# Performance work log

Hardware: AMD Instinct MI355X
Metric: run time of the kernel (lower is better)

## Reference

```python
import jax, jax.numpy as jnp
import numpy as np

SCALE = 0.5
DROP_P = 0.2

def setup_inputs() -> dict:
    key = jax.random.key(0)
    k1, k2 = jax.random.split(key)
    x1 = jax.random.normal(k1, (8, 2048, 128), dtype=jnp.float32)
    x2 = jax.random.normal(k2, (8, 2048, 128), dtype=jnp.float32)
    return {"x1": x1, "x2": x2}

def reference(x1, x2):
    # scores: [B, M, N] = x1 @ x2^T, scaled by 0.5
    scores = jnp.einsum('bmd,bnd->bmn', x1, x2) * SCALE
    probs = jax.nn.softmax(scores, axis=-1)
    # dropout p=0.2 (training mode in the torch source); fixed key for determinism
    keep = jax.random.bernoulli(jax.random.key(42), 1.0 - DROP_P, probs.shape)
    probs = jnp.where(keep, probs / (1.0 - DROP_P), 0.0)
    # out: [B, M, D] = probs @ x2
    return jnp.einsum('bmn,bnd->bmd', probs, x2)
```

## Files before the change

### kernel.cpp

```cpp
#include <hip/hip_runtime.h>
#include <stdint.h>


typedef __bf16 bf16x8 __attribute__((ext_vector_type(8)));
typedef float f32x4 __attribute__((ext_vector_type(4)));

union FragAB {
  bf16x8 v;
  uint32_t u[4];
};

__device__ __forceinline__ uint32_t rotl32(uint32_t x, uint32_t r) {
  return (x << r) | (x >> (32u - r));
}

__device__ __forceinline__ void threefry2x32_k42(uint32_t in0, uint32_t in1,
                                                 uint32_t& o0, uint32_t& o1) {
  const uint32_t ks0 = 0u;
  const uint32_t ks1 = 42u;
  const uint32_t ks2 = 0x1BD11BDAu ^ 0u ^ 42u;
  uint32_t x0 = in0 + ks0;
  uint32_t x1 = in1 + ks1;
#define TFR(r) { x0 += x1; x1 = rotl32(x1, r); x1 ^= x0; }
  TFR(13u) TFR(15u) TFR(26u) TFR(6u)
  x0 += ks1; x1 += ks2 + 1u;
  TFR(17u) TFR(29u) TFR(16u) TFR(24u)
  x0 += ks2; x1 += ks0 + 2u;
  TFR(13u) TFR(15u) TFR(26u) TFR(6u)
  x0 += ks0; x1 += ks1 + 3u;
  TFR(17u) TFR(29u) TFR(16u) TFR(24u)
  x0 += ks1; x1 += ks2 + 4u;
  TFR(13u) TFR(15u) TFR(26u) TFR(6u)
  x0 += ks2; x1 += ks0 + 5u;
#undef TFR
  o0 = x0; o1 = x1;
}

__device__ __forceinline__ uint32_t pack_bf16(float a, float b) {
  __bf16 ba = (__bf16)a;
  __bf16 bb = (__bf16)b;
  uint32_t ua = (uint32_t)__builtin_bit_cast(uint16_t, ba);
  uint32_t ub = (uint32_t)__builtin_bit_cast(uint16_t, bb);
  return ua | (ub << 16);
}

#define KEEP_LT 3435974144u
#define MBIAS 40.0f

__launch_bounds__(256, 4)
__global__ void prep_kernel(const float* __restrict__ x2,
                            uint4* __restrict__ KF,
                            uint4* __restrict__ VF) {
  const int tid = threadIdx.x;
  const int w = tid >> 6;
  const int lane = tid & 63;
  const int l15 = lane & 15;
  const int g = lane >> 4;
  const int T = blockIdx.x;
  const int b = blockIdx.y;
  const float* xb = x2 + (size_t)b * 2048 * 128;

  #pragma unroll
  for (int h = 0; h < 2; ++h) {
    const int n = T * 32 + h * 16 + l15;
    const float* p = xb + (size_t)n * 128 + w * 32 + 8 * g;
    float4 f0 = *(const float4*)(p);
    float4 f1 = *(const float4*)(p + 4);
    uint4 u;
    u.x = pack_bf16(f0.x, f0.y);
    u.y = pack_bf16(f0.z, f0.w);
    u.z = pack_bf16(f1.x, f1.y);
    u.w = pack_bf16(f1.z, f1.w);
    KF[(size_t)((b * 64 + T) * 8 + w * 2 + h) * 64 + lane] = u;
  }

  #pragma unroll
  for (int i = 0; i < 2; ++i) {
    const int dt = w + 4 * i;
    const int d = dt * 16 + l15;
    const float* p = xb + (size_t)(T * 32 + 8 * g) * 128 + d;
    uint4 u;
    u.x = pack_bf16(p[0],   p[128]);
    u.y = pack_bf16(p[256], p[384]);
    u.z = pack_bf16(p[512], p[640]);
    u.w = pack_bf16(p[768], p[896]);
    VF[(size_t)((b * 64 + T) * 8 + dt) * 64 + lane] = u;
  }
}

__launch_bounds__(256, 4)
__global__ void attn2_kernel(const float* __restrict__ x1,
                             const uint4* __restrict__ KF,
                             const uint4* __restrict__ VF,
                             float* __restrict__ out) {
  __shared__ __attribute__((aligned(16))) uint32_t SMEM[8768];

  const int tid = threadIdx.x;
  const int w = __builtin_amdgcn_readfirstlane(tid >> 6);
  const int lane = tid & 63;
  const int l15 = lane & 15;
  const int g = lane >> 4;
  const int id = blockIdx.y * 128 + blockIdx.x;
  const int b = id & 7;
  const int m0 = (id >> 3) * 16;

  uint32_t* PbW = &SMEM[w * 320];

  const float QSCALE = 0.5f * 1.44269504088896340736f;
  FragAB qf[4];
  {
    const float* qp_base = x1 + ((size_t)b * 2048 + m0 + l15) * 128;
    #pragma unroll
    for (int c = 0; c < 4; ++c) {
      const float* qp = qp_base + c * 32 + g * 8;
      float4 f0 = *(const float4*)(qp);
      float4 f1 = *(const float4*)(qp + 4);
      qf[c].u[0] = pack_bf16(f0.x * QSCALE, f0.y * QSCALE);
      qf[c].u[1] = pack_bf16(f0.z * QSCALE, f0.w * QSCALE);
      qf[c].u[2] = pack_bf16(f1.x * QSCALE, f1.y * QSCALE);
      qf[c].u[3] = pack_bf16(f1.z * QSCALE, f1.w * QSCALE);
    }
  }

  f32x4 o[8];
  #pragma unroll
  for (int dt = 0; dt < 8; ++dt) o[dt] = (f32x4){0.f, 0.f, 0.f, 0.f};
  float lsum = 0.f;

  const uint32_t rb = (uint32_t)b * 4194304u +
                      (uint32_t)(m0 + l15) * 2048u + (uint32_t)(w * 512);

  const uint4* kfp = KF + (size_t)((b * 64 + w * 16) * 8) * 64 + lane;
  const uint4* vfp = VF + (size_t)((b * 64 + w * 16) * 8) * 64 + lane;

  uint4 kf[8], vf[8];
  #pragma unroll
  for (int i = 0; i < 8; ++i) kf[i] = kfp[i * 64];

  for (int tile = 0; tile < 16; ++tile) {
    f32x4 sa[2];
    sa[0] = (f32x4){0.f, 0.f, 0.f, 0.f};
    sa[1] = (f32x4){0.f, 0.f, 0.f, 0.f};
    #pragma unroll
    for (int c = 0; c < 4; ++c) {
      FragAB k0, k1;
      k0.u[0] = kf[2 * c].x; k0.u[1] = kf[2 * c].y;
      k0.u[2] = kf[2 * c].z; k0.u[3] = kf[2 * c].w;
      k1.u[0] = kf[2 * c + 1].x; k1.u[1] = kf[2 * c + 1].y;
      k1.u[2] = kf[2 * c + 1].z; k1.u[3] = kf[2 * c + 1].w;
      sa[0] = __builtin_amdgcn_mfma_f32_16x16x32_bf16(k0.v, qf[c].v, sa[0], 0, 0, 0);
      sa[1] = __builtin_amdgcn_mfma_f32_16x16x32_bf16(k1.v, qf[c].v, sa[1], 0, 0, 0);
    }

    #pragma unroll
    for (int i = 0; i < 8; ++i) vf[i] = vfp[i * 64];
    kfp += 512;
    #pragma unroll
    for (int i = 0; i < 8; ++i) kf[i] = kfp[i * 64];

    #pragma unroll
    for (int t = 0; t < 2; ++t) {
      float p0 = __builtin_amdgcn_exp2f(sa[t][0] - MBIAS);
      float p1 = __builtin_amdgcn_exp2f(sa[t][1] - MBIAS);
      float p2 = __builtin_amdgcn_exp2f(sa[t][2] - MBIAS);
      float p3 = __builtin_amdgcn_exp2f(sa[t][3] - MBIAS);
      lsum += (p0 + p1) + (p2 + p3);
      uint32_t ib = rb + (uint32_t)(tile * 32 + t * 16 + 4 * g);
      uint32_t h0, h1, bits;
      threefry2x32_k42(0u, ib + 0u, h0, h1); bits = h0 ^ h1;
      float q0 = (bits < KEEP_LT) ? p0 : 0.0f;
      threefry2x32_k42(0u, ib + 1u, h0, h1); bits = h0 ^ h1;
      float q1 = (bits < KEEP_LT) ? p1 : 0.0f;
      threefry2x32_k42(0u, ib + 2u, h0, h1); bits = h0 ^ h1;
      float q2 = (bits < KEEP_LT) ? p2 : 0.0f;
      threefry2x32_k42(0u, ib + 3u, h0, h1); bits = h0 ^ h1;
      float q3 = (bits < KEEP_LT) ? p3 : 0.0f;
      *(uint2*)&PbW[l15 * 20 + t * 8 + 2 * g] =
          make_uint2(pack_bf16(q0, q1), pack_bf16(q2, q3));
    }
    asm volatile("s_waitcnt lgkmcnt(0)" ::: "memory");
    FragAB pa;
    {
      uint4 pu = *(const uint4*)&PbW[l15 * 20 + 4 * g];
      pa.u[0] = pu.x; pa.u[1] = pu.y; pa.u[2] = pu.z; pa.u[3] = pu.w;
    }

    #pragma unroll
    for (int dt = 0; dt < 8; ++dt) {
      FragAB vb;
      vb.u[0] = vf[dt].x; vb.u[1] = vf[dt].y;
      vb.u[2] = vf[dt].z; vb.u[3] = vf[dt].w;
      o[dt] = __builtin_amdgcn_mfma_f32_16x16x32_bf16(pa.v, vb.v, o[dt], 0, 0, 0);
    }
    vfp += 512;
  }

  __syncthreads();
  float* EP = (float*)&SMEM[0];
  float* EPL = EP + 8192;
  EPL[l15 * 36 + w * 4 + g] = lsum;
  #pragma unroll
  for (int dt = 0; dt < 8; ++dt)
    #pragma unroll
    for (int r = 0; r < 4; ++r)
      EP[((w * 8 + dt) * 4 + r) * 64 + lane] = o[dt][r];
  __syncthreads();
  float scale[4];
  #pragma unroll
  for (int r = 0; r < 4; ++r) {
    const float4* lp = (const float4*)&EPL[(4 * g + r) * 36];
    float4 A = lp[0], B4 = lp[1], C4 = lp[2], D4 = lp[3];
    float L = ((A.x + A.y) + (A.z + A.w)) + ((B4.x + B4.y) + (B4.z + B4.w)) +
              ((C4.x + C4.y) + (C4.z + C4.w)) + ((D4.x + D4.y) + (D4.z + D4.w));
    scale[r] = 1.0f / (L * 0.8f);
  }
  #pragma unroll
  for (int i = 0; i < 2; ++i) {
    const int dt = w * 2 + i;
    #pragma unroll
    for (int r = 0; r < 4; ++r) {
      int base = (dt * 4 + r) * 64 + lane;
      float tot = EP[base] + EP[base + 2048] + EP[base + 4096] + EP[base + 6144];
      out[((size_t)b * 2048 + m0 + 4 * g + r) * 128 + dt * 16 + l15] =
          tot * scale[r];
    }
  }
}

__launch_bounds__(256, 2)
__global__ void attn_kernel(const float* __restrict__ x1,
                            const float* __restrict__ x2,
                            float* __restrict__ out) {
  __shared__ __attribute__((aligned(16))) uint32_t SMEM[4][4800];

  const int tid = threadIdx.x;
  const int wv = __builtin_amdgcn_readfirstlane(tid >> 6);
  const int lane = tid & 63;
  const int l15 = lane & 15;
  const int g = lane >> 4;
  const int b = blockIdx.y;
  const int m0 = blockIdx.x * 32;

  uint32_t* KtW = &SMEM[wv][0];
  uint32_t* VtW = &SMEM[wv][2176];
  uint32_t* PbW = &SMEM[wv][4480];

  const float QSCALE = 0.5f * 1.44269504088896340736f;
  FragAB qf[2][4];
  #pragma unroll
  for (int s = 0; s < 2; ++s) {
    const float* qp_base = x1 + ((size_t)b * 2048 + m0 + s * 16 + l15) * 128;
    #pragma unroll
    for (int c = 0; c < 4; ++c) {
      const float* qp = qp_base + c * 32 + g * 8;
      float4 f0 = *(const float4*)(qp);
      float4 f1 = *(const float4*)(qp + 4);
      qf[s][c].u[0] = pack_bf16(f0.x * QSCALE, f0.y * QSCALE);
      qf[s][c].u[1] = pack_bf16(f0.z * QSCALE, f0.w * QSCALE);
      qf[s][c].u[2] = pack_bf16(f1.x * QSCALE, f1.y * QSCALE);
      qf[s][c].u[3] = pack_bf16(f1.z * QSCALE, f1.w * QSCALE);
    }
  }

  f32x4 o[2][8];
  #pragma unroll
  for (int s = 0; s < 2; ++s)
    #pragma unroll
    for (int dt = 0; dt < 8; ++dt) o[s][dt] = (f32x4){0.f, 0.f, 0.f, 0.f};
  float lsum[2] = {0.f, 0.f};

  uint32_t rb[2];
  #pragma unroll
  for (int s = 0; s < 2; ++s)
    rb[s] = (uint32_t)b * 4194304u +
            (uint32_t)(m0 + s * 16 + l15) * 2048u + (uint32_t)(wv * 512);

  const float4* x2b4 = (const float4*)(x2 + (size_t)b * 2048 * 128);
  const uint32_t permsel = (l15 & 1) ? 0x07060302u : 0x05040100u;

  for (int tile = 0; tile < 16; ++tile) {
    const int n0g = wv * 512 + tile * 32;

    #pragma unroll
    for (int i = 0; i < 16; ++i) {
      int n = 2 * i + (lane >> 5);
      int dq = lane & 31;
      float4 v = x2b4[(size_t)(n0g + n) * 32 + dq];
      uint32_t p0 = pack_bf16(v.x, v.y);
      uint32_t p1 = pack_bf16(v.z, v.w);
      *(uint2*)&KtW[n * 68 + 2 * dq] = make_uint2(p0, p1);
      VtW[dq * 36 + n] = p0;
      VtW[(dq + 32) * 36 + n] = p1;
    }
    asm volatile("s_waitcnt lgkmcnt(0)" ::: "memory");

    f32x4 sa[2][2];
    #pragma unroll
    for (int s = 0; s < 2; ++s)
      #pragma unroll
      for (int t = 0; t < 2; ++t) sa[s][t] = (f32x4){0.f, 0.f, 0.f, 0.f};
    #pragma unroll
    for (int c = 0; c < 4; ++c) {
      FragAB k0, k1;
      uint4 a0 = *(const uint4*)&KtW[l15 * 68 + c * 16 + 4 * g];
      uint4 a1 = *(const uint4*)&KtW[(16 + l15) * 68 + c * 16 + 4 * g];
      k0.u[0] = a0.x; k0.u[1] = a0.y; k0.u[2] = a0.z; k0.u[3] = a0.w;
      k1.u[0] = a1.x; k1.u[1] = a1.y; k1.u[2] = a1.z; k1.u[3] = a1.w;
      sa[0][0] = __builtin_amdgcn_mfma_f32_16x16x32_bf16(k0.v, qf[0][c].v, sa[0][0], 0, 0, 0);
      sa[0][1] = __builtin_amdgcn_mfma_f32_16x16x32_bf16(k1.v, qf[0][c].v, sa[0][1], 0, 0, 0);
      sa[1][0] = __builtin_amdgcn_mfma_f32_16x16x32_bf16(k0.v, qf[1][c].v, sa[1][0], 0, 0, 0);
      sa[1][1] = __builtin_amdgcn_mfma_f32_16x16x32_bf16(k1.v, qf[1][c].v, sa[1][1], 0, 0, 0);
    }

    FragAB pa[2];
    #pragma unroll
    for (int s = 0; s < 2; ++s) {
      #pragma unroll
      for (int t = 0; t < 2; ++t) {
        float p0 = __builtin_amdgcn_exp2f(sa[s][t][0] - MBIAS);
        float p1 = __builtin_amdgcn_exp2f(sa[s][t][1] - MBIAS);
        float p2 = __builtin_amdgcn_exp2f(sa[s][t][2] - MBIAS);
        float p3 = __builtin_amdgcn_exp2f(sa[s][t][3] - MBIAS);
        lsum[s] += (p0 + p1) + (p2 + p3);
        uint32_t ib = rb[s] + (uint32_t)(tile * 32 + t * 16 + 4 * g);
        uint32_t h0, h1, bits;
        threefry2x32_k42(0u, ib + 0u, h0, h1); bits = h0 ^ h1;
        float q0 = (bits < KEEP_LT) ? p0 : 0.0f;
        threefry2x32_k42(0u, ib + 1u, h0, h1); bits = h0 ^ h1;
        float q1 = (bits < KEEP_LT) ? p1 : 0.0f;
        threefry2x32_k42(0u, ib + 2u, h0, h1); bits = h0 ^ h1;
        float q2 = (bits < KEEP_LT) ? p2 : 0.0f;
        threefry2x32_k42(0u, ib + 3u, h0, h1); bits = h0 ^ h1;
        float q3 = (bits < KEEP_LT) ? p3 : 0.0f;
        *(uint2*)&PbW[l15 * 20 + t * 8 + 2 * g] =
            make_uint2(pack_bf16(q0, q1), pack_bf16(q2, q3));
      }
      asm volatile("s_waitcnt lgkmcnt(0)" ::: "memory");
      uint4 pu = *(const uint4*)&PbW[l15 * 20 + 4 * g];
      pa[s].u[0] = pu.x; pa[s].u[1] = pu.y; pa[s].u[2] = pu.z; pa[s].u[3] = pu.w;
    }

    #pragma unroll
    for (int dt = 0; dt < 8; ++dt) {
      int rowp = ((l15 >> 1) & 1) * 32 + 4 * dt + (l15 >> 2);
      const uint32_t* vr = &VtW[rowp * 36 + 8 * g];
      uint4 U0 = *(const uint4*)vr;
      uint4 U1 = *(const uint4*)(vr + 4);
      FragAB vb;
      vb.u[0] = __builtin_amdgcn_perm(U0.y, U0.x, permsel);
      vb.u[1] = __builtin_amdgcn_perm(U0.w, U0.z, permsel);
      vb.u[2] = __builtin_amdgcn_perm(U1.y, U1.x, permsel);
      vb.u[3] = __builtin_amdgcn_perm(U1.w, U1.z, permsel);
      o[0][dt] = __builtin_amdgcn_mfma_f32_16x16x32_bf16(pa[0].v, vb.v, o[0][dt], 0, 0, 0);
      o[1][dt] = __builtin_amdgcn_mfma_f32_16x16x32_bf16(pa[1].v, vb.v, o[1][dt], 0, 0, 0);
    }
  }

  __syncthreads();
  float* EP = (float*)&SMEM[0][0];
  #pragma unroll
  for (int s = 0; s < 2; ++s) {
    #pragma unroll
    for (int dt = 0; dt < 8; ++dt)
      #pragma unroll
      for (int r = 0; r < 4; ++r)
        EP[(((wv * 2 + s) * 8 + dt) * 4 + r) * 64 + lane] = o[s][dt][r];
    EP[16384 + (s * 16 + l15) * 16 + wv * 4 + g] = lsum[s];
  }
  __syncthreads();
  const int s = wv >> 1;
  float scale[4];
  #pragma unroll
  for (int r = 0; r < 4; ++r) {
    const float4* lp = (const float4*)&EP[16384 + (s * 16 + 4 * g + r) * 16];
    float4 A = lp[0], B4 = lp[1], C4 = lp[2], D4 = lp[3];
    float L = ((A.x + A.y) + (A.z + A.w)) + ((B4.x + B4.y) + (B4.z + B4.w)) +
              ((C4.x + C4.y) + (C4.z + C4.w)) + ((D4.x + D4.y) + (D4.z + D4.w));
    scale[r] = 1.0f / (L * 0.8f);
  }
  #pragma unroll
  for (int it = 0; it < 4; ++it) {
    int dt = (wv * 4 + it) & 7;
    #pragma unroll
    for (int r = 0; r < 4; ++r) {
      int base = ((s * 8 + dt) * 4 + r) * 64 + lane;
      float tot = EP[base] + EP[base + 4096] + EP[base + 8192] + EP[base + 12288];
      out[((size_t)b * 2048 + m0 + s * 16 + 4 * g + r) * 128 + dt * 16 + l15] =
          tot * scale[r];
    }
  }
}

extern "C" void kernel_launch(void* const* d_in, const int* in_sizes, int n_in,
                              void* d_out, int out_size, void* d_ws, size_t ws_size,
                              hipStream_t stream) {
  const float* x1 = (const float*)d_in[0];
  const float* x2 = (const float*)d_in[1];
  float* out = (float*)d_out;
  if (d_ws != nullptr && ws_size >= (size_t)8 * 1024 * 1024) {
    uint4* KF = (uint4*)d_ws;
    uint4* VF = KF + 262144;
    prep_kernel<<<dim3(64, 8, 1), dim3(256, 1, 1), 0, stream>>>(x2, KF, VF);
    attn2_kernel<<<dim3(128, 8, 1), dim3(256, 1, 1), 0, stream>>>(x1, KF, VF, out);
  } else {
    attn_kernel<<<dim3(64, 8, 1), dim3(256, 1, 1), 0, stream>>>(x1, x2, out);
  }
}
```

Baseline: 148.0 us.

## Precompute next tile's dropout mask and drop explicit K/V register prefetch

Moves the threefry dropout-mask generation for the next tile into the current iteration and stores it as float multipliers, so the hash ALU work can overlap with MFMA and memory latency. K and V fragments are now loaded directly inside the MFMA loops instead of being software-prefetched into register arrays, which lowers register pressure but leaves load scheduling to the compiler. The MBIAS subtraction before exp2 is removed, which assumes the scaled scores stay small enough not to overflow. Union-based fragment packing is replaced with bit casts.

```diff
diff --git a/kernel.cpp b/kernel.cpp
--- a/kernel.cpp
+++ b/kernel.cpp
@@ -4,11 +4,6 @@
 
 typedef __bf16 bf16x8 __attribute__((ext_vector_type(8)));
 typedef float f32x4 __attribute__((ext_vector_type(4)));
-
-union FragAB {
-  bf16x8 v;
-  uint32_t u[4];
-};
 
 __device__ __forceinline__ uint32_t rotl32(uint32_t x, uint32_t r) {
   return (x << r) | (x >> (32u - r));
@@ -107,7 +102,7 @@
   uint32_t* PbW = &SMEM[w * 320];
 
   const float QSCALE = 0.5f * 1.44269504088896340736f;
-  FragAB qf[4];
+  bf16x8 qfv[4];
   {
     const float* qp_base = x1 + ((size_t)b * 2048 + m0 + l15) * 128;
     #pragma unroll
@@ -115,10 +110,12 @@
       const float* qp = qp_base + c * 32 + g * 8;
       float4 f0 = *(const float4*)(qp);
       float4 f1 = *(const float4*)(qp + 4);
-      qf[c].u[0] = pack_bf16(f0.x * QSCALE, f0.y * QSCALE);
-      qf[c].u[1] = pack_bf16(f0.z * QSCALE, f0.w * QSCALE);
-      qf[c].u[2] = pack_bf16(f1.x * QSCALE, f1.y * QSCALE);
-      qf[c].u[3] = pack_bf16(f1.z * QSCALE, f1.w * QSCALE);
+      uint4 u;
+      u.x = pack_bf16(f0.x * QSCALE, f0.y * QSCALE);
+      u.y = pack_bf16(f0.z * QSCALE, f0.w * QSCALE);
+      u.z = pack_bf16(f1.x * QSCALE, f1.y * QSCALE);
+      u.w = pack_bf16(f1.z * QSCALE, f1.w * QSCALE);
+      qfv[c] = __builtin_bit_cast(bf16x8, u);
     }
   }
 
@@ -127,15 +124,24 @@
   for (int dt = 0; dt < 8; ++dt) o[dt] = (f32x4){0.f, 0.f, 0.f, 0.f};
   float lsum = 0.f;
 
-  const uint32_t rb = (uint32_t)b * 4194304u +
-                      (uint32_t)(m0 + l15) * 2048u + (uint32_t)(w * 512);
+  const uint32_t rbg = (uint32_t)b * 4194304u +
+                       (uint32_t)(m0 + l15) * 2048u + (uint32_t)(w * 512) +
+                       (uint32_t)(4 * g);
 
   const uint4* kfp = KF + (size_t)((b * 64 + w * 16) * 8) * 64 + lane;
   const uint4* vfp = VF + (size_t)((b * 64 + w * 16) * 8) * 64 + lane;
 
-  uint4 kf[8], vf[8];
-  #pragma unroll
-  for (int i = 0; i < 8; ++i) kf[i] = kfp[i * 64];
+  float mcur[8], mnext[8];
+  #pragma unroll
+  for (int j = 0; j < 8; ++j) mnext[j] = 0.f;
+  #pragma unroll
+  for (int t = 0; t < 2; ++t)
+    #pragma unroll
+    for (int r = 0; r < 4; ++r) {
+      uint32_t h0, h1;
+      threefry2x32_k42(0u, rbg + (uint32_t)(t * 16 + r), h0, h1);
+      mcur[t * 4 + r] = ((h0 ^ h1) < KEEP_LT) ? 1.0f : 0.0f;
+    }
 
   for (int tile = 0; tile < 16; ++tile) {
     f32x4 sa[2];
@@ -143,55 +149,52 @@
     sa[1] = (f32x4){0.f, 0.f, 0.f, 0.f};
     #pragma unroll
     for (int c = 0; c < 4; ++c) {
-      FragAB k0, k1;
-      k0.u[0] = kf[2 * c].x; k0.u[1] = kf[2 * c].y;
-      k0.u[2] = kf[2 * c].z; k0.u[3] = kf[2 * c].w;
-      k1.u[0] = kf[2 * c + 1].x; k1.u[1] = kf[2 * c + 1].y;
-      k1.u[2] = kf[2 * c + 1].z; k1.u[3] = kf[2 * c + 1].w;
-      sa[0] = __builtin_amdgcn_mfma_f32_16x16x32_bf16(k0.v, qf[c].v, sa[0], 0, 0, 0);
-      sa[1] = __builtin_amdgcn_mfma_f32_16x16x32_bf16(k1.v, qf[c].v, sa[1], 0, 0, 0);
-    }
-
-    #pragma unroll
-    for (int i = 0; i < 8; ++i) vf[i] = vfp[i * 64];
-    kfp += 512;
-    #pragma unroll
-    for (int i = 0; i < 8; ++i) kf[i] = kfp[i * 64];
+      bf16x8 k0 = __builtin_bit_cast(bf16x8, kfp[(c * 2 + 0) * 64]);
+      bf16x8 k1 = __builtin_bit_cast(bf16x8, kfp[(c * 2 + 1) * 64]);
+      sa[0] = __builtin_amdgcn_mfma_f32_16x16x32_bf16(k0, qfv[c], sa[0], 0, 0, 0);
+      sa[1] = __builtin_amdgcn_mfma_f32_16x16x32_bf16(k1, qfv[c], sa[1], 0, 0, 0);
+    }
 
     #pragma unroll
     for (int t = 0; t < 2; ++t) {
-      float p0 = __builtin_amdgcn_exp2f(sa[t][0] - MBIAS);
-      float p1 = __builtin_amdgcn_exp2f(sa[t][1] - MBIAS);
-      float p2 = __builtin_amdgcn_exp2f(sa[t][2] - MBIAS);
-      float p3 = __builtin_amdgcn_exp2f(sa[t][3] - MBIAS);
+      float p0 = __builtin_amdgcn_exp2f(sa[t][0]);
+      float p1 = __builtin_amdgcn_exp2f(sa[t][1]);
+      float p2 = __builtin_amdgcn_exp2f(sa[t][2]);
+      float p3 = __builtin_amdgcn_exp2f(sa[t][3]);
       lsum += (p0 + p1) + (p2 + p3);
-      uint32_t ib = rb + (uint32_t)(tile * 32 + t * 16 + 4 * g);
-      uint32_t h0, h1, bits;
-      threefry2x32_k42(0u, ib + 0u, h0, h1); bits = h0 ^ h1;
-      float q0 = (bits < KEEP_LT) ? p0 : 0.0f;
-      threefry2x32_k42(0u, ib + 1u, h0, h1); bits = h0 ^ h1;
-      float q1 = (bits < KEEP_LT) ? p1 : 0.0f;
-      threefry2x32_k42(0u, ib + 2u, h0, h1); bits = h0 ^ h1;
-      float q2 = (bits < KEEP_LT) ? p2 : 0.0f;
-      threefry2x32_k42(0u, ib + 3u, h0, h1); bits = h0 ^ h1;
-      float q3 = (bits < KEEP_LT) ? p3 : 0.0f;
+      float q0 = p0 * mcur[t * 4 + 0];
+      float q1 = p1 * mcur[t * 4 + 1];
+      float q2 = p2 * mcur[t * 4 + 2];
+      float q3 = p3 * mcur[t * 4 + 3];
       *(uint2*)&PbW[l15 * 20 + t * 8 + 2 * g] =
           make_uint2(pack_bf16(q0, q1), pack_bf16(q2, q3));
     }
+
+    if (tile < 15) {
+      const uint32_t base = rbg + (uint32_t)((tile + 1) * 32);
+      #pragma unroll
+      for (int t = 0; t < 2; ++t)
+        #pragma unroll
+        for (int r = 0; r < 4; ++r) {
+          uint32_t h0, h1;
+          threefry2x32_k42(0u, base + (uint32_t)(t * 16 + r), h0, h1);
+          mnext[t * 4 + r] = ((h0 ^ h1) < KEEP_LT) ? 1.0f : 0.0f;
+        }
+    }
+
     asm volatile("s_waitcnt lgkmcnt(0)" ::: "memory");
-    FragAB pa;
-    {
-      uint4 pu = *(const uint4*)&PbW[l15 * 20 + 4 * g];
-      pa.u[0] = pu.x; pa.u[1] = pu.y; pa.u[2] = pu.z; pa.u[3] = pu.w;
-    }
+    uint4 pu = *(const uint4*)&PbW[l15 * 20 + 4 * g];
+    bf16x8 pav = __builtin_bit_cast(bf16x8, pu);
 
     #pragma unroll
     for (int dt = 0; dt < 8; ++dt) {
-      FragAB vb;
-      vb.u[0] = vf[dt].x; vb.u[1] = vf[dt].y;
-      vb.u[2] = vf[dt].z; vb.u[3] = vf[dt].w;
-      o[dt] = __builtin_amdgcn_mfma_f32_16x16x32_bf16(pa.v, vb.v, o[dt], 0, 0, 0);
-    }
+      bf16x8 vb = __builtin_bit_cast(bf16x8, vfp[dt * 64]);
+      o[dt] = __builtin_amdgcn_mfma_f32_16x16x32_bf16(pav, vb, o[dt], 0, 0, 0);
+    }
+
+    #pragma unroll
+    for (int j = 0; j < 8; ++j) mcur[j] = mnext[j];
+    kfp += 512;
     vfp += 512;
   }
 
@@ -222,10 +225,15 @@
       int base = (dt * 4 + r) * 64 + lane;
       float tot = EP[base] + EP[base + 2048] + EP[base + 4096] + EP[base + 6144];
       out[((size_t)b * 2048 + m0 + 4 * g + r) * 128 + dt * 16 + l15] =
-          tot * scale[r];
-    }
-  }
-}
+          tot * scale[i == 0 ? r : r];
+    }
+  }
+}
+
+union FragAB {
+  bf16x8 v;
+  uint32_t u[4];
+};
 
 __launch_bounds__(256, 2)
 __global__ void attn_kernel(const float* __restrict__ x1,
```

Result: no change. 147.3 us (-0.5%).
